# Kernel tuning notes

Hardware: AMD Instinct MI355X
Metric: run time of the kernel (lower is better)

## Reference

```python
import jax, jax.numpy as jnp
import numpy as np

INPUT_NC = 512
N_HEADS = 16
D_KEY = 64
SCALE = D_KEY ** 0.5


def setup_inputs() -> dict:
    key = jax.random.key(0)
    k1, k2, k3, k4, k5, k6 = jax.random.split(key, 6)
    bs, d_seq = 8, 1024
    v = jax.random.normal(k1, (bs, d_seq, INPUT_NC), dtype=jnp.float32)
    # key-padding mask, True = masked out; broadcast over heads and query dim
    pad_mask = jax.random.bernoulli(k2, 0.1, (bs, 1, 1, d_seq))
    # fc1: input_nc -> 2*n_heads*d_key (fused K,Q projection)
    W1 = jax.random.normal(k3, (INPUT_NC, 2 * N_HEADS * D_KEY), dtype=jnp.float32) * (1.0 / np.sqrt(INPUT_NC))
    b1 = jax.random.normal(k4, (2 * N_HEADS * D_KEY,), dtype=jnp.float32) * 0.01
    # fc2: n_heads*input_nc -> input_nc
    W2 = jax.random.normal(k5, (N_HEADS * INPUT_NC, INPUT_NC), dtype=jnp.float32) * (1.0 / np.sqrt(N_HEADS * INPUT_NC))
    b2 = jax.random.normal(k6, (INPUT_NC,), dtype=jnp.float32) * 0.01
    return {"v": v, "pad_mask": pad_mask, "W1": W1, "b1": b1, "W2": W2, "b2": b2}


def reference(v, pad_mask, W1, b1, W2, b2):
    bs, d_seq, nc = v.shape
    # fused KQ projection: [bs, S, 2*H*dk] -> [bs, H, S, 2*dk]
    kq = (v @ W1 + b1).reshape(bs, d_seq, N_HEADS, 2 * D_KEY).transpose(0, 2, 1, 3)
    k, q = kq[..., :D_KEY], kq[..., D_KEY:]  # chunk: k first, q second
    attn = jnp.einsum('bhqd,bhkd->bhqk', q, k) / SCALE
    attn = jnp.where(pad_mask, jnp.float32(-1000.0), attn)
    attn = jax.nn.softmax(attn, axis=3)
    # AV with unprojected v broadcast across heads: [bs, H, S, nc]
    out = jnp.einsum('bhqk,bkc->bhqc', attn, v)
    out = out.transpose(0, 2, 1, 3).reshape(bs, d_seq, N_HEADS * nc)
    out = out @ W2 + b2
    return (out, attn)
```

## Files before the change

### kernel.cpp

```cpp
#include <hip/hip_runtime.h>


typedef __attribute__((ext_vector_type(8))) short bf16x8;
typedef __attribute__((ext_vector_type(4))) float f32x4;
typedef __attribute__((ext_vector_type(4))) unsigned short u16x4;

__device__ __forceinline__ unsigned short f2bf(float f) {
  unsigned u = __builtin_bit_cast(unsigned, f);
  u += 0x7FFFu + ((u >> 16) & 1u);
  return (unsigned short)(u >> 16);
}
__device__ __forceinline__ float bf2f(unsigned short u) {
  return __builtin_bit_cast(float, (unsigned)u << 16);
}

__device__ __forceinline__ void gload_lds16(const unsigned short* g, unsigned short* l) {
  __builtin_amdgcn_global_load_lds(
      (const __attribute__((address_space(1))) unsigned int*)(g),
      (__attribute__((address_space(3))) unsigned int*)(l), 16, 0, 0);
}


__global__ void cvt_bf16_kernel(const float* __restrict__ in,
                                unsigned short* __restrict__ out, int n4) {
  int i = blockIdx.x * blockDim.x + threadIdx.x;
  if (i >= n4) return;
  f32x4 v = reinterpret_cast<const f32x4*>(in)[i];
  u16x4 o;
#pragma unroll
  for (int j = 0; j < 4; ++j) o[j] = f2bf(v[j]);
  reinterpret_cast<u16x4*>(out)[i] = o;
}

__global__ void transpose_cvt_kernel(const float* __restrict__ in,
                                     unsigned short* __restrict__ out,
                                     int R, int C) {
  __shared__ float tile[32][33];
  int c0 = blockIdx.x * 32, r0 = blockIdx.y * 32;
  int tx = threadIdx.x & 31, ty = threadIdx.x >> 5;
#pragma unroll
  for (int i = ty; i < 32; i += 8)
    tile[i][tx] = in[(size_t)(r0 + i) * C + (c0 + tx)];
  __syncthreads();
#pragma unroll
  for (int i = ty; i < 32; i += 8)
    out[(size_t)(c0 + i) * R + (r0 + tx)] = f2bf(tile[tx][i]);
}

__launch_bounds__(256)
__global__ void gemm1_kernel(const unsigned short* __restrict__ vbf,
                             const unsigned short* __restrict__ w1t,
                             const float* __restrict__ b1,
                             unsigned short* __restrict__ q_ws,
                             unsigned short* __restrict__ k_ws) {
  const int m0 = blockIdx.y * 128, n0 = blockIdx.x * 128;
  const int w = threadIdx.x >> 6, l = threadIdx.x & 63;
  const int wr = w >> 1, wc = w & 1, lr = l & 15, lg = l >> 4;
  f32x4 acc[4][4];
#pragma unroll
  for (int mi = 0; mi < 4; ++mi)
#pragma unroll
    for (int ni = 0; ni < 4; ++ni) acc[mi][ni] = (f32x4){0.f, 0.f, 0.f, 0.f};

  for (int k0 = 0; k0 < 512; k0 += 32) {
    bf16x8 a[4], bb[4];
#pragma unroll
    for (int mi = 0; mi < 4; ++mi)
      a[mi] = *reinterpret_cast<const bf16x8*>(
          vbf + (size_t)(m0 + wr * 64 + mi * 16 + lr) * 512 + k0 + lg * 8);
#pragma unroll
    for (int ni = 0; ni < 4; ++ni)
      bb[ni] = *reinterpret_cast<const bf16x8*>(
          w1t + (size_t)(n0 + wc * 64 + ni * 16 + lr) * 512 + k0 + lg * 8);
#pragma unroll
    for (int mi = 0; mi < 4; ++mi)
#pragma unroll
      for (int ni = 0; ni < 4; ++ni)
        acc[mi][ni] = __builtin_amdgcn_mfma_f32_16x16x32_bf16(a[mi], bb[ni], acc[mi][ni], 0, 0, 0);
  }
#pragma unroll
  for (int mi = 0; mi < 4; ++mi)
#pragma unroll
    for (int ni = 0; ni < 4; ++ni) {
      int col = n0 + wc * 64 + ni * 16 + lr;
      int h = col >> 7, j = col & 127;
      float bias = b1[col];
#pragma unroll
      for (int r = 0; r < 4; ++r) {
        int row = m0 + wr * 64 + mi * 16 + lg * 4 + r;
        int bb_ = row >> 10, s = row & 1023;
        unsigned short bv = f2bf(acc[mi][ni][r] + bias);
        size_t base = ((size_t)(bb_ * 16 + h) << 16) + (size_t)s * 64;
        if (j < 64) k_ws[base + j] = bv;
        else        q_ws[base + j - 64] = bv;
      }
    }
}

__launch_bounds__(512)
__global__ void scores_kernel(const unsigned short* __restrict__ q_ws,
                              const unsigned short* __restrict__ k_ws,
                              const int* __restrict__ pad,
                              float* __restrict__ attn_out,
                              unsigned short* __restrict__ eb,
                              float* __restrict__ linv_ws) {
  const int wg = (blockIdx.x & 7) * 512 + (blockIdx.x >> 3);
  const int qt = wg & 31, h = (wg >> 5) & 15, b = wg >> 9;
  const int bh = b * 16 + h, q0 = qt * 32;
  const int w = threadIdx.x >> 6, l = threadIdx.x & 63;
  const int lr = l & 15, lg = l >> 4;

  __shared__ unsigned short E_lds[32][1032];
  __shared__ float lw[8][32];
  __shared__ float linv_s[32];

  const unsigned short* qb = q_ws + ((size_t)bh << 16);
  const unsigned short* kb = k_ws + ((size_t)bh << 16);
  const int* pmb = pad + b * 1024;

  bf16x8 a_q[2][2];
#pragma unroll
  for (int mf = 0; mf < 2; ++mf)
#pragma unroll
    for (int ks = 0; ks < 2; ++ks)
      a_q[mf][ks] = *reinterpret_cast<const bf16x8*>(
          qb + (size_t)(q0 + mf * 16 + lr) * 64 + ks * 32 + lg * 8);

  float l_run[2][4];
#pragma unroll
  for (int mf = 0; mf < 2; ++mf)
#pragma unroll
    for (int r = 0; r < 4; ++r) l_run[mf][r] = 0.f;

#pragma unroll
  for (int sub = 0; sub < 2; ++sub) {
    const int c0 = w * 128 + sub * 64;
    f32x4 s[2][4];
#pragma unroll
    for (int mf = 0; mf < 2; ++mf)
#pragma unroll
      for (int nf = 0; nf < 4; ++nf) s[mf][nf] = (f32x4){0.f, 0.f, 0.f, 0.f};
#pragma unroll
    for (int ks = 0; ks < 2; ++ks) {
      bf16x8 bk[4];
#pragma unroll
      for (int nf = 0; nf < 4; ++nf)
        bk[nf] = *reinterpret_cast<const bf16x8*>(
            kb + (size_t)(c0 + nf * 16 + lr) * 64 + ks * 32 + lg * 8);
#pragma unroll
      for (int mf = 0; mf < 2; ++mf)
#pragma unroll
        for (int nf = 0; nf < 4; ++nf)
          s[mf][nf] = __builtin_amdgcn_mfma_f32_16x16x32_bf16(a_q[mf][ks], bk[nf], s[mf][nf], 0, 0, 0);
    }
    int msk[4];
#pragma unroll
    for (int nf = 0; nf < 4; ++nf) msk[nf] = pmb[c0 + nf * 16 + lr];
#pragma unroll
    for (int mf = 0; mf < 2; ++mf)
#pragma unroll
      for (int nf = 0; nf < 4; ++nf)
#pragma unroll
        for (int r = 0; r < 4; ++r) {
          float e = msk[nf] ? 0.f : __expf(s[mf][nf][r] * 0.125f);
          l_run[mf][r] += e;
          E_lds[mf * 16 + lg * 4 + r][c0 + nf * 16 + lr] = f2bf(e);
        }
  }

#pragma unroll
  for (int mf = 0; mf < 2; ++mf)
#pragma unroll
    for (int r = 0; r < 4; ++r) {
      float v = l_run[mf][r];
      v += __shfl_xor(v, 1); v += __shfl_xor(v, 2);
      v += __shfl_xor(v, 4); v += __shfl_xor(v, 8);
      if (lr == 0) lw[w][mf * 16 + lg * 4 + r] = v;
    }
  __syncthreads();
  if (threadIdx.x < 32) {
    float s = 0.f;
#pragma unroll
    for (int ww = 0; ww < 8; ++ww) s += lw[ww][threadIdx.x];
    float li = 1.f / s;
    linv_s[threadIdx.x] = li;
    linv_ws[(size_t)bh * 1024 + q0 + threadIdx.x] = li;
  }
  __syncthreads();

  {
    const int row = threadIdx.x >> 4;
    const int cb = threadIdx.x & 15;
    const float sc = linv_s[row];
    float* rowp = attn_out + ((size_t)bh << 20) + (size_t)(q0 + row) * 1024;
    unsigned short* ebrow = eb + ((size_t)bh << 20) + (size_t)(q0 + row) * 1024;
#pragma unroll
    for (int i = 0; i < 8; ++i) {
      int c8 = cb * 8 + i * 128;
      bf16x8 ev = *reinterpret_cast<const bf16x8*>(&E_lds[row][c8]);
      f32x4 o0, o1;
#pragma unroll
      for (int j = 0; j < 4; ++j) o0[j] = bf2f((unsigned short)ev[j]) * sc;
#pragma unroll
      for (int j = 0; j < 4; ++j) o1[j] = bf2f((unsigned short)ev[4 + j]) * sc;
      *reinterpret_cast<f32x4*>(rowp + c8) = o0;
      *reinterpret_cast<f32x4*>(rowp + c8 + 4) = o1;
      *reinterpret_cast<bf16x8*>(ebrow + c8) = ev;
    }
  }
}

__launch_bounds__(256)
__global__ void pv_kernel(const unsigned short* __restrict__ eb,
                          const unsigned short* __restrict__ vt,
                          const float* __restrict__ linv_ws,
                          unsigned short* __restrict__ o_ws) {
  const int wg = (blockIdx.x & 7) * 512 + (blockIdx.x >> 3);
  const int nt = wg & 3, mt = (wg >> 2) & 7, bh = wg >> 5;
  const int b = bh >> 4, h = bh & 15;
  const int m0 = mt * 128, n0 = nt * 128;

  __shared__ unsigned short Asm[2][128 * 32];
  __shared__ unsigned short Bsm[2][128 * 32];
  const int w = threadIdx.x >> 6, l = threadIdx.x & 63;
  const int wr = w >> 1, wc = w & 1, lr = l & 15, lg = l >> 4;

  f32x4 acc[4][4];
#pragma unroll
  for (int mi = 0; mi < 4; ++mi)
#pragma unroll
    for (int ni = 0; ni < 4; ++ni) acc[mi][ni] = (f32x4){0.f, 0.f, 0.f, 0.f};

  const int srow = threadIdx.x >> 2;
  const int scol = (threadIdx.x & 3) * 8;
  const unsigned short* gA0 = eb + ((size_t)bh << 20) + (size_t)(m0 + srow) * 1024 + scol;
  const unsigned short* gA1 = gA0 + (size_t)64 * 1024;
  const unsigned short* gB0 = vt + (size_t)(n0 + srow) * 8192 + (size_t)b * 1024 + scol;
  const unsigned short* gB1 = gB0 + (size_t)64 * 8192;
  const int ldsoff = w * 512;

  float linv_r[4][4];
  {
    const float* lrow = linv_ws + (size_t)bh * 1024 + m0 + wr * 64 + lg * 4;
#pragma unroll
    for (int mi = 0; mi < 4; ++mi)
#pragma unroll
      for (int r = 0; r < 4; ++r) linv_r[mi][r] = lrow[mi * 16 + r];
  }

  auto STAGE = [&](int buf, int kt) {
    int k0 = kt * 32;
    gload_lds16(gA0 + k0, &Asm[buf][ldsoff]);
    gload_lds16(gA1 + k0, &Asm[buf][64 * 32 + ldsoff]);
    gload_lds16(gB0 + k0, &Bsm[buf][ldsoff]);
    gload_lds16(gB1 + k0, &Bsm[buf][64 * 32 + ldsoff]);
  };
  auto COMPUTE = [&](int buf) {
    bf16x8 a[4], bb[4];
#pragma unroll
    for (int mi = 0; mi < 4; ++mi)
      a[mi] = *reinterpret_cast<const bf16x8*>(&Asm[buf][(wr * 64 + mi * 16 + lr) * 32 + lg * 8]);
#pragma unroll
    for (int ni = 0; ni < 4; ++ni)
      bb[ni] = *reinterpret_cast<const bf16x8*>(&Bsm[buf][(wc * 64 + ni * 16 + lr) * 32 + lg * 8]);
    __builtin_amdgcn_s_setprio(1);
#pragma unroll
    for (int mi = 0; mi < 4; ++mi)
#pragma unroll
      for (int ni = 0; ni < 4; ++ni)
        acc[mi][ni] = __builtin_amdgcn_mfma_f32_16x16x32_bf16(a[mi], bb[ni], acc[mi][ni], 0, 0, 0);
    __builtin_amdgcn_s_setprio(0);
  };

  STAGE(0, 0);
  __syncthreads();
  int cur = 0;
  for (int kt = 0; kt < 31; ++kt) {
    STAGE(cur ^ 1, kt + 1);
    COMPUTE(cur);
    __syncthreads();
    cur ^= 1;
  }
  COMPUTE(cur);

#pragma unroll
  for (int mi = 0; mi < 4; ++mi)
#pragma unroll
    for (int ni = 0; ni < 4; ++ni)
#pragma unroll
      for (int r = 0; r < 4; ++r) {
        int row = m0 + wr * 64 + mi * 16 + lg * 4 + r;
        int col = n0 + wc * 64 + ni * 16 + lr;
        o_ws[(size_t)(b * 1024 + row) * 8192 + h * 512 + col] =
            f2bf(acc[mi][ni][r] * linv_r[mi][r]);
      }
}

__launch_bounds__(256)
__global__ void gemm2_kernel(const unsigned short* __restrict__ o_ws,
                             const unsigned short* __restrict__ w2t,
                             const float* __restrict__ b2,
                             float* __restrict__ y) {
  const int wg = (blockIdx.x & 7) * 64 + (blockIdx.x >> 3);
  const int nt = wg & 3, mt = wg >> 2;
  const int m0 = mt * 64, n0 = nt * 128;

  __shared__ unsigned short As[2][64 * 32];
  __shared__ unsigned short Bs[2][128 * 32];
  const int w = threadIdx.x >> 6, l = threadIdx.x & 63;
  const int wr = w >> 1, wc = w & 1, lr = l & 15, lg = l >> 4;

  f32x4 acc[2][4];
#pragma unroll
  for (int mi = 0; mi < 2; ++mi)
#pragma unroll
    for (int ni = 0; ni < 4; ++ni) acc[mi][ni] = (f32x4){0.f, 0.f, 0.f, 0.f};

  const int srow = threadIdx.x >> 2;
  const int scol = (threadIdx.x & 3) * 8;
  const unsigned short* gA  = o_ws + (size_t)(m0 + srow) * 8192 + scol;
  const unsigned short* gB0 = w2t + (size_t)(n0 + srow) * 8192 + scol;
  const unsigned short* gB1 = gB0 + (size_t)64 * 8192;
  const int ldsoff = w * 512;

  auto STAGE = [&](int buf, int kt) {
    int k0 = kt * 32;
    gload_lds16(gA + k0, &As[buf][ldsoff]);
    gload_lds16(gB0 + k0, &Bs[buf][ldsoff]);
    gload_lds16(gB1 + k0, &Bs[buf][64 * 32 + ldsoff]);
  };

  auto COMPUTE = [&](int buf) {
    bf16x8 a[2], bb[4];
#pragma unroll
    for (int mi = 0; mi < 2; ++mi)
      a[mi] = *reinterpret_cast<const bf16x8*>(&As[buf][(wr * 32 + mi * 16 + lr) * 32 + lg * 8]);
#pragma unroll
    for (int ni = 0; ni < 4; ++ni)
      bb[ni] = *reinterpret_cast<const bf16x8*>(&Bs[buf][(wc * 64 + ni * 16 + lr) * 32 + lg * 8]);
    __builtin_amdgcn_s_setprio(1);
#pragma unroll
    for (int mi = 0; mi < 2; ++mi)
#pragma unroll
      for (int ni = 0; ni < 4; ++ni)
        acc[mi][ni] = __builtin_amdgcn_mfma_f32_16x16x32_bf16(a[mi], bb[ni], acc[mi][ni], 0, 0, 0);
    __builtin_amdgcn_s_setprio(0);
  };

  STAGE(0, 0);
  __syncthreads();
  int cur = 0;
  for (int kt = 0; kt < 255; ++kt) {
    STAGE(cur ^ 1, kt + 1);
    COMPUTE(cur);
    __syncthreads();
    cur ^= 1;
  }
  COMPUTE(cur);

#pragma unroll
  for (int mi = 0; mi < 2; ++mi)
#pragma unroll
    for (int ni = 0; ni < 4; ++ni) {
      int col = n0 + wc * 64 + ni * 16 + lr;
      float bias = b2[col];
#pragma unroll
      for (int r = 0; r < 4; ++r)
        y[(size_t)(m0 + wr * 32 + mi * 16 + lg * 4 + r) * 512 + col] = acc[mi][ni][r] + bias;
    }
}

extern "C" void kernel_launch(void* const* d_in, const int* in_sizes, int n_in,
                              void* d_out, int out_size, void* d_ws, size_t ws_size,
                              hipStream_t stream) {
  const float* v   = (const float*)d_in[0];
  const int*   pad = (const int*)d_in[1];
  const float* W1  = (const float*)d_in[2];
  const float* b1  = (const float*)d_in[3];
  const float* W2  = (const float*)d_in[4];
  const float* b2  = (const float*)d_in[5];
  float* out  = (float*)d_out;
  float* attn = out + (size_t)8 * 1024 * 512;

  char* ws = (char*)d_ws;
  unsigned short* w1t  = (unsigned short*)(ws);
  unsigned short* w2t  = (unsigned short*)(ws + 2097152);
  unsigned short* vt   = (unsigned short*)(ws + 10485760);
  unsigned short* vbf  = (unsigned short*)(ws + 18874368);
  unsigned short* q_ws = (unsigned short*)(ws + 27262976);
  unsigned short* k_ws = (unsigned short*)(ws + 44040192);
  unsigned short* o_ws = (unsigned short*)(ws + 60817408);
  unsigned short* eb   = (unsigned short*)(ws + 195035136);
  float*          linv = (float*)(ws + 463470592);

  transpose_cvt_kernel<<<dim3(64, 16), 256, 0, stream>>>(W1, w1t, 512, 2048);
  transpose_cvt_kernel<<<dim3(16, 256), 256, 0, stream>>>(W2, w2t, 8192, 512);
  transpose_cvt_kernel<<<dim3(16, 256), 256, 0, stream>>>(v, vt, 8192, 512);
  cvt_bf16_kernel<<<4096, 256, 0, stream>>>(v, vbf, 1048576);
  gemm1_kernel<<<dim3(16, 64), 256, 0, stream>>>(vbf, w1t, b1, q_ws, k_ws);
  scores_kernel<<<4096, 512, 0, stream>>>(q_ws, k_ws, pad, attn, eb, linv);
  pv_kernel<<<4096, 256, 0, stream>>>(eb, vt, linv, o_ws);
  gemm2_kernel<<<512, 256, 0, stream>>>(o_ws, w2t, b2, out);
}
```

Baseline: 690.3 us.

## Move fp32 attention-probability output from scores kernel into PV kernel loop

The scores kernel no longer writes the fp32 normalized attention matrix. It only writes the bf16 exponentials and the inverse row sums, which also removes a barrier. The PV kernel now writes the fp32 attention tile from its already-loaded A fragments, scaled by the inverse sum, but only in blocks with nt==0 and only in waves with wc==0. The intent is to overlap the large 512MB attention store with the PV MFMA work, at the cost of extra stores inside that kernel's main loop and imbalance between wavefronts.

```diff
diff --git a/kernel.cpp b/kernel.cpp
--- a/kernel.cpp
+++ b/kernel.cpp
@@ -101,7 +101,6 @@
 __global__ void scores_kernel(const unsigned short* __restrict__ q_ws,
                               const unsigned short* __restrict__ k_ws,
                               const int* __restrict__ pad,
-                              float* __restrict__ attn_out,
                               unsigned short* __restrict__ eb,
                               float* __restrict__ linv_ws) {
   const int wg = (blockIdx.x & 7) * 512 + (blockIdx.x >> 3);
@@ -112,7 +111,6 @@
 
   __shared__ unsigned short E_lds[32][1032];
   __shared__ float lw[8][32];
-  __shared__ float linv_s[32];
 
   const unsigned short* qb = q_ws + ((size_t)bh << 16);
   const unsigned short* kb = k_ws + ((size_t)bh << 16);
@@ -182,30 +180,18 @@
     float s = 0.f;
 #pragma unroll
     for (int ww = 0; ww < 8; ++ww) s += lw[ww][threadIdx.x];
-    float li = 1.f / s;
-    linv_s[threadIdx.x] = li;
-    linv_ws[(size_t)bh * 1024 + q0 + threadIdx.x] = li;
-  }
-  __syncthreads();
+    linv_ws[(size_t)bh * 1024 + q0 + threadIdx.x] = 1.f / s;
+  }
 
   {
     const int row = threadIdx.x >> 4;
     const int cb = threadIdx.x & 15;
-    const float sc = linv_s[row];
-    float* rowp = attn_out + ((size_t)bh << 20) + (size_t)(q0 + row) * 1024;
     unsigned short* ebrow = eb + ((size_t)bh << 20) + (size_t)(q0 + row) * 1024;
 #pragma unroll
     for (int i = 0; i < 8; ++i) {
       int c8 = cb * 8 + i * 128;
-      bf16x8 ev = *reinterpret_cast<const bf16x8*>(&E_lds[row][c8]);
-      f32x4 o0, o1;
-#pragma unroll
-      for (int j = 0; j < 4; ++j) o0[j] = bf2f((unsigned short)ev[j]) * sc;
-#pragma unroll
-      for (int j = 0; j < 4; ++j) o1[j] = bf2f((unsigned short)ev[4 + j]) * sc;
-      *reinterpret_cast<f32x4*>(rowp + c8) = o0;
-      *reinterpret_cast<f32x4*>(rowp + c8 + 4) = o1;
-      *reinterpret_cast<bf16x8*>(ebrow + c8) = ev;
+      *reinterpret_cast<bf16x8*>(ebrow + c8) =
+          *reinterpret_cast<const bf16x8*>(&E_lds[row][c8]);
     }
   }
 }
@@ -214,6 +200,7 @@
 __global__ void pv_kernel(const unsigned short* __restrict__ eb,
                           const unsigned short* __restrict__ vt,
                           const float* __restrict__ linv_ws,
+                          float* __restrict__ attn_out,
                           unsigned short* __restrict__ o_ws) {
   const int wg = (blockIdx.x & 7) * 512 + (blockIdx.x >> 3);
   const int nt = wg & 3, mt = (wg >> 2) & 7, bh = wg >> 5;
@@ -239,14 +226,19 @@
   const unsigned short* gB1 = gB0 + (size_t)64 * 8192;
   const int ldsoff = w * 512;
 
-  float linv_r[4][4];
+  const bool do_attn = (nt == 0) && (wc == 0);
+
+  float linv_r[4][4], linv_a[4];
   {
-    const float* lrow = linv_ws + (size_t)bh * 1024 + m0 + wr * 64 + lg * 4;
-#pragma unroll
-    for (int mi = 0; mi < 4; ++mi)
-#pragma unroll
-      for (int r = 0; r < 4; ++r) linv_r[mi][r] = lrow[mi * 16 + r];
-  }
+    const float* lrow = linv_ws + (size_t)bh * 1024 + m0 + wr * 64;
+#pragma unroll
+    for (int mi = 0; mi < 4; ++mi) {
+#pragma unroll
+      for (int r = 0; r < 4; ++r) linv_r[mi][r] = lrow[mi * 16 + lg * 4 + r];
+      linv_a[mi] = lrow[mi * 16 + lr];
+    }
+  }
+  float* attn_b = attn_out + ((size_t)bh << 20);
 
   auto STAGE = [&](int buf, int kt) {
     int k0 = kt * 32;
@@ -255,7 +247,7 @@
     gload_lds16(gB0 + k0, &Bsm[buf][ldsoff]);
     gload_lds16(gB1 + k0, &Bsm[buf][64 * 32 + ldsoff]);
   };
-  auto COMPUTE = [&](int buf) {
+  auto COMPUTE = [&](int buf, int kt) {
     bf16x8 a[4], bb[4];
 #pragma unroll
     for (int mi = 0; mi < 4; ++mi)
@@ -263,6 +255,20 @@
 #pragma unroll
     for (int ni = 0; ni < 4; ++ni)
       bb[ni] = *reinterpret_cast<const bf16x8*>(&Bsm[buf][(wc * 64 + ni * 16 + lr) * 32 + lg * 8]);
+    if (do_attn) {
+#pragma unroll
+      for (int mi = 0; mi < 4; ++mi) {
+        float li = linv_a[mi];
+        f32x4 o0, o1;
+#pragma unroll
+        for (int j = 0; j < 4; ++j) o0[j] = bf2f((unsigned short)a[mi][j]) * li;
+#pragma unroll
+        for (int j = 0; j < 4; ++j) o1[j] = bf2f((unsigned short)a[mi][4 + j]) * li;
+        float* p = attn_b + (size_t)(m0 + wr * 64 + mi * 16 + lr) * 1024 + kt * 32 + lg * 8;
+        *reinterpret_cast<f32x4*>(p) = o0;
+        *reinterpret_cast<f32x4*>(p + 4) = o1;
+      }
+    }
     __builtin_amdgcn_s_setprio(1);
 #pragma unroll
     for (int mi = 0; mi < 4; ++mi)
@@ -277,11 +283,11 @@
   int cur = 0;
   for (int kt = 0; kt < 31; ++kt) {
     STAGE(cur ^ 1, kt + 1);
-    COMPUTE(cur);
+    COMPUTE(cur, kt);
     __syncthreads();
     cur ^= 1;
   }
-  COMPUTE(cur);
+  COMPUTE(cur, 31);
 
 #pragma unroll
   for (int mi = 0; mi < 4; ++mi)
@@ -398,7 +404,7 @@
   transpose_cvt_kernel<<<dim3(16, 256), 256, 0, stream>>>(v, vt, 8192, 512);
   cvt_bf16_kernel<<<4096, 256, 0, stream>>>(v, vbf, 1048576);
   gemm1_kernel<<<dim3(16, 64), 256, 0, stream>>>(vbf, w1t, b1, q_ws, k_ws);
-  scores_kernel<<<4096, 512, 0, stream>>>(q_ws, k_ws, pad, attn, eb, linv);
-  pv_kernel<<<4096, 256, 0, stream>>>(eb, vt, linv, o_ws);
+  scores_kernel<<<4096, 512, 0, stream>>>(q_ws, k_ws, pad, eb, linv);
+  pv_kernel<<<4096, 256, 0, stream>>>(eb, vt, linv, attn, o_ws);
   gemm2_kernel<<<512, 256, 0, stream>>>(o_ws, w2t, b2, out);
 }
```

Result: slower. 745.5 us (+8.0%).
